# Optimization experiments

Measured on AMD Instinct MI355X. Metric: run time of the kernel, lower is better.

The kernel has to match this reference:

```python
import jax, jax.numpy as jnp
import numpy as np

N = 50000        # nodes
E = 800000       # edges (avg degree 16)
D_IN = 64
D_HID = 128      # 2 * out_dim
D_OUT = 64


def setup_inputs() -> dict:
    key = jax.random.key(0)
    ks = jax.random.split(key, 6)
    x = jax.random.normal(ks[0], (N, D_IN), dtype=jnp.float32)
    edge_index = jax.random.randint(ks[1], (2, E), 0, N, dtype=jnp.int32)
    # Glorot-style init like PyG GCNConv
    W1 = jax.random.normal(ks[2], (D_IN, D_HID), dtype=jnp.float32) / np.sqrt(D_IN)
    b1 = jnp.zeros((D_HID,), dtype=jnp.float32)
    W2 = jax.random.normal(ks[3], (D_HID, D_OUT), dtype=jnp.float32) / np.sqrt(D_HID)
    b2 = jnp.zeros((D_OUT,), dtype=jnp.float32)
    return {"x": x, "edge_index": edge_index, "W1": W1, "b1": b1, "W2": W2, "b2": b2}


def _gcn_norm(edge_index, num_nodes):
    # PyG GCNConv default: add self-loops, symmetric normalization D^-1/2 A_hat D^-1/2
    loop = jnp.arange(num_nodes, dtype=edge_index.dtype)
    src = jnp.concatenate([edge_index[0], loop])
    dst = jnp.concatenate([edge_index[1], loop])
    deg = jax.ops.segment_sum(jnp.ones_like(dst, dtype=jnp.float32), dst,
                              num_segments=num_nodes)
    dinv = jnp.where(deg > 0, jax.lax.rsqrt(deg), 0.0)
    norm = dinv[src] * dinv[dst]  # [E+N]
    return src, dst, norm


def _gcn_conv(x, W, b, src, dst, norm, num_nodes):
    h = x @ W                                      # [N, F_out]
    msg = h[src] * norm[:, None]                   # gather + scale, [E+N, F_out]
    out = jax.ops.segment_sum(msg, dst, num_segments=num_nodes)  # scatter-add
    return out + b


def reference(x, edge_index, W1, b1, W2, b2):
    num_nodes = x.shape[0]
    src, dst, norm = _gcn_norm(edge_index, num_nodes)
    h = _gcn_conv(x, W1, b1, src, dst, norm, num_nodes)
    h = jax.nn.relu(h)
    node_emb = _gcn_conv(h, W2, b2, src, dst, norm, num_nodes)
    return node_emb
```

## Files before the change

kernel.cpp:

```cpp
#include <hip/hip_runtime.h>

typedef unsigned short u16;
typedef unsigned int u32;

typedef __attribute__((ext_vector_type(8))) short bf16x8;
typedef __attribute__((ext_vector_type(4))) float f32x4;

#define BSH 8
#define CAP 5120
#define OVFCAP 8192
#define CHUNK 2048

__device__ __forceinline__ float bf2f(u16 u) {
    return __uint_as_float(((u32)u) << 16);
}
__device__ __forceinline__ u16 f2bf(float f) {
    u32 x = __float_as_uint(f);
    return (u16)((x + 0x7fffu + ((x >> 16) & 1u)) >> 16);
}

__device__ __forceinline__ bool block_isbf(const u16* __restrict__ x, float* sflag) {
    int tid = threadIdx.x;
    if (tid < 64) {
        u16 v = x[tid * 2];
        u32 ex = (v >> 7) & 0xFFu;
        unsigned long long m = __ballot(ex >= 90u && ex <= 140u);
        if (tid == 0) *sflag = (m == ~0ull) ? 1.0f : 0.0f;
    }
    __syncthreads();
    return *sflag != 0.0f;
}

__device__ __forceinline__ void acc8(uint4 w, float* a) {
    a[0] += bf2f((u16)(w.x & 0xFFFFu)); a[1] += bf2f((u16)(w.x >> 16));
    a[2] += bf2f((u16)(w.y & 0xFFFFu)); a[3] += bf2f((u16)(w.y >> 16));
    a[4] += bf2f((u16)(w.z & 0xFFFFu)); a[5] += bf2f((u16)(w.z >> 16));
    a[6] += bf2f((u16)(w.w & 0xFFFFu)); a[7] += bf2f((u16)(w.w >> 16));
}

__device__ __forceinline__ u32 scale2(u32 g, float di) {
    u16 lo = f2bf(bf2f((u16)(g & 0xFFFFu)) * di);
    u16 hi = f2bf(bf2f((u16)(g >> 16)) * di);
    return (u32)lo | ((u32)hi << 16);
}

__global__ __launch_bounds__(256) void k_binA2(
    const int* __restrict__ src, const int* __restrict__ dst,
    int* __restrict__ gcur, u32* __restrict__ staging,
    u32* __restrict__ ovf, int* __restrict__ ovfcur, int E) {
    __shared__ int hcnt[256];
    __shared__ int hbase[256];
    const int tid = threadIdx.x;
    const int e0 = blockIdx.x * CHUNK;
    const int e1 = min(e0 + CHUNK, E);
    hcnt[tid] = 0;
    __syncthreads();
    int dl[8], sl[8];
#pragma unroll
    for (int k = 0; k < 8; k++) {
        int e = e0 + tid + k * 256;
        bool ok = e < e1;
        dl[k] = ok ? dst[e] : -1;
        sl[k] = ok ? src[e] : 0;
        if (ok) atomicAdd(&hcnt[dl[k] >> BSH], 1);
    }
    __syncthreads();
    {
        int c = hcnt[tid];
        hbase[tid] = (c > 0) ? atomicAdd(&gcur[tid], c) : 0;
        hcnt[tid] = 0;
    }
    __syncthreads();
#pragma unroll
    for (int k = 0; k < 8; k++) {
        int d = dl[k];
        if (d < 0) continue;
        int b = d >> BSH;
        int r = atomicAdd(&hcnt[b], 1);
        int p = hbase[b] + r;
        if (p < CAP) {
            staging[(size_t)b * CAP + p] = (u32)sl[k] | ((u32)(d & 255) << 16);
        } else {
            int q = atomicAdd(ovfcur, 1);
            if (q < OVFCAP) ovf[q] = (u32)sl[k] | ((u32)d << 16);
        }
    }
}

__global__ __launch_bounds__(256) void k_bucket(
    const u32* __restrict__ staging, const int* __restrict__ gcur,
    const u32* __restrict__ ovf, const int* __restrict__ ovfcur,
    int* __restrict__ row_start, float* __restrict__ dinv,
    u16* __restrict__ csr, int nbuck,
    const void* __restrict__ W1, const void* __restrict__ b1,
    const void* __restrict__ W2, const void* __restrict__ b2,
    u16* __restrict__ wc,
    const void* __restrict__ x, u16* __restrict__ gxt, int N, int E) {
    __shared__ float sflag;
    __shared__ int hcnt[256];
    __shared__ int hscan[256];
    __shared__ int hcur[256];
    __shared__ int sred[256];
    __shared__ int sbase;
    __shared__ float sdinv[256];
    const int bid = blockIdx.x;
    const int tid = threadIdx.x;
    bool isbf = block_isbf((const u16*)x, &sflag);

    if (bid < nbuck) {
        const int b = bid;
        const int used = min(gcur[b], CAP);
        const u32* st = staging + (size_t)b * CAP;
        const int no = min(ovfcur[0], OVFCAP);
        const int used4 = used >> 2;
        sred[tid] = (tid < b) ? gcur[tid] : 0;
        hcnt[tid] = 0;
        __syncthreads();
        for (int s = 128; s > 0; s >>= 1) {
            if (tid < s) sred[tid] += sred[tid + s];
            __syncthreads();
        }
        if (tid == 0) sbase = sred[0];
        for (int i = tid; i < used4; i += 256) {
            uint4 p4 = ((const uint4*)st)[i];
            atomicAdd(&hcnt[p4.x >> 16], 1);
            atomicAdd(&hcnt[p4.y >> 16], 1);
            atomicAdd(&hcnt[p4.z >> 16], 1);
            atomicAdd(&hcnt[p4.w >> 16], 1);
        }
        for (int i = (used4 << 2) + tid; i < used; i += 256)
            atomicAdd(&hcnt[st[i] >> 16], 1);
        for (int i = tid; i < no; i += 256) {
            u32 pk = ovf[i];
            int d = (int)(pk >> 16);
            if ((d >> BSH) == b) atomicAdd(&hcnt[d & 255], 1);
        }
        __syncthreads();
        int v = hcnt[tid];
        hscan[tid] = v;
        __syncthreads();
        for (int s = 1; s < 256; s <<= 1) {
            int t = (tid >= s) ? hscan[tid - s] : 0;
            __syncthreads();
            hscan[tid] += t;
            __syncthreads();
        }
        int excl = hscan[tid] - v;
        hcur[tid] = excl;
        int base = sbase;
        float dv = rsqrtf((float)(v + 1));
        sdinv[tid] = dv;
        int node = (b << BSH) + tid;
        if (node < N) {
            row_start[node] = base + excl;
            dinv[node] = dv;
        }
        if (b == 0 && tid == 0) row_start[N] = E;
        __syncthreads();
        for (int i = tid; i < used4; i += 256) {
            uint4 p4 = ((const uint4*)st)[i];
            int r0 = atomicAdd(&hcur[p4.x >> 16], 1); csr[base + r0] = (u16)(p4.x & 0xFFFFu);
            int r1 = atomicAdd(&hcur[p4.y >> 16], 1); csr[base + r1] = (u16)(p4.y & 0xFFFFu);
            int r2 = atomicAdd(&hcur[p4.z >> 16], 1); csr[base + r2] = (u16)(p4.z & 0xFFFFu);
            int r3 = atomicAdd(&hcur[p4.w >> 16], 1); csr[base + r3] = (u16)(p4.w & 0xFFFFu);
        }
        for (int i = (used4 << 2) + tid; i < used; i += 256) {
            u32 pk = st[i];
            int r = atomicAdd(&hcur[pk >> 16], 1);
            csr[base + r] = (u16)(pk & 0xFFFFu);
        }
        for (int i = tid; i < no; i += 256) {
            u32 pk = ovf[i];
            int d = (int)(pk >> 16);
            if ((d >> BSH) == b) {
                int r = atomicAdd(&hcur[d & 255], 1);
                csr[base + r] = (u16)(pk & 0xFFFFu);
            }
        }
        const int row0 = b << BSH;
        for (int i = tid; i < 256 * 16; i += 256) {
            int rl = i >> 4;
            int node2 = row0 + rl;
            if (node2 >= N) break;
            int q = i & 15;
            size_t idx = (size_t)node2 * 16 + q;
            float di = sdinv[rl];
            float4 vv;
            if (isbf) {
                ushort4 u = ((const ushort4*)x)[idx];
                vv.x = bf2f(u.x); vv.y = bf2f(u.y); vv.z = bf2f(u.z); vv.w = bf2f(u.w);
            } else {
                vv = ((const float4*)x)[idx];
            }
            ushort4 o;
            o.x = f2bf(vv.x * di); o.y = f2bf(vv.y * di);
            o.z = f2bf(vv.z * di); o.w = f2bf(vv.w * di);
            ((ushort4*)gxt)[idx] = o;
        }
    } else {
        int cb = bid - nbuck;
        for (int i = cb * 256 + tid; i < 16576; i += 17 * 256) {
            const void* s; int off;
            if (i < 8192)       { int nn = i >> 6, k = i & 63;  s = W1; off = k * 128 + nn; }
            else if (i < 16384) { int j = i - 8192; int nn = j >> 7, k = j & 127; s = W2; off = k * 64 + nn; }
            else if (i < 16512) { s = b1; off = i - 16384; }
            else                { s = b2; off = i - 16512; }
            wc[i] = isbf ? ((const u16*)s)[off] : f2bf(((const float*)s)[off]);
        }
    }
}

template<bool FINAL>
__global__ __launch_bounds__(256) void k_gather(
    const uint4* __restrict__ feat, const int* __restrict__ row_start,
    const u16* __restrict__ csr, const float* __restrict__ dinv,
    const u16* __restrict__ b2c, const void* __restrict__ xdet,
    void* __restrict__ outp, int n) {
    __shared__ float sflag;
    bool isbf = true;
    if (FINAL) isbf = block_isbf((const u16*)xdet, &sflag);
    int t = blockIdx.x * 256 + threadIdx.x;
    int d = t >> 3;
    int lane = t & 7;
    if (d >= n) return;
    const uint4* fl = feat + lane;
    float a[8];
    {
        uint4 w = fl[(size_t)d * 8];
        a[0] = bf2f((u16)(w.x & 0xFFFFu)); a[1] = bf2f((u16)(w.x >> 16));
        a[2] = bf2f((u16)(w.y & 0xFFFFu)); a[3] = bf2f((u16)(w.y >> 16));
        a[4] = bf2f((u16)(w.z & 0xFFFFu)); a[5] = bf2f((u16)(w.z >> 16));
        a[6] = bf2f((u16)(w.w & 0xFFFFu)); a[7] = bf2f((u16)(w.w >> 16));
    }
    int s0 = row_start[d], s1 = row_start[d + 1];
    int deg = s1 - s0;
    int j = s0;
    int end8 = s0 + (deg & ~7);
    for (; j < end8; j += 8) {
        int idx = (int)csr[j + lane];
        uint4 wv[8];
#pragma unroll
        for (int u = 0; u < 8; u++) {
            int sv = __shfl(idx, u, 8);
            wv[u] = fl[(size_t)sv * 8];
        }
#pragma unroll
        for (int u = 0; u < 8; u++) acc8(wv[u], a);
    }
    int rem = s1 - j;
    if (rem > 0) {
        int idx = (lane < rem) ? (int)csr[j + lane] : 0;
        for (int u = 0; u < rem; u++) {
            int sv = __shfl(idx, u, 8);
            uint4 wv = fl[(size_t)sv * 8];
            acc8(wv, a);
        }
    }
    if (FINAL) {
        float di = dinv[d];
#pragma unroll
        for (int u = 0; u < 8; u++)
            a[u] = a[u] * di + bf2f(b2c[8 * lane + u]);
        if (isbf) {
            uint4 o;
            o.x = (u32)f2bf(a[0]) | ((u32)f2bf(a[1]) << 16);
            o.y = (u32)f2bf(a[2]) | ((u32)f2bf(a[3]) << 16);
            o.z = (u32)f2bf(a[4]) | ((u32)f2bf(a[5]) << 16);
            o.w = (u32)f2bf(a[6]) | ((u32)f2bf(a[7]) << 16);
            ((uint4*)outp)[(size_t)d * 8 + lane] = o;
        } else {
            float4* op = (float4*)outp;
            op[(size_t)d * 16 + 2 * lane]     = make_float4(a[0], a[1], a[2], a[3]);
            op[(size_t)d * 16 + 2 * lane + 1] = make_float4(a[4], a[5], a[6], a[7]);
        }
    } else {
        uint4 o;
        o.x = (u32)f2bf(a[0]) | ((u32)f2bf(a[1]) << 16);
        o.y = (u32)f2bf(a[2]) | ((u32)f2bf(a[3]) << 16);
        o.z = (u32)f2bf(a[4]) | ((u32)f2bf(a[5]) << 16);
        o.w = (u32)f2bf(a[6]) | ((u32)f2bf(a[7]) << 16);
        ((uint4*)outp)[(size_t)d * 8 + lane] = o;
    }
}

__global__ __launch_bounds__(256) void k_mlp(
    const u16* __restrict__ accin, const u16* __restrict__ wc,
    const float* __restrict__ dinv, u16* outb, int n) {
    __shared__ __align__(16) u16 As[32 * 72];
    __shared__ __align__(16) u16 W1t[128 * 72];
    __shared__ __align__(16) u16 W2t[64 * 136];
    __shared__ __align__(16) u16 Hs[32 * 136];
    __shared__ float b1s[128];
    __shared__ float dvs[32];
    const int tid = threadIdx.x;
    const int row0 = blockIdx.x * 32;

    if (tid < 32) {
        int r = row0 + tid;
        dvs[tid] = (r < n) ? dinv[r] : 0.f;
    } else if (tid < 160) {
        b1s[tid - 32] = bf2f(wc[16384 + tid - 32]);
    }
    {
        int i = tid;
        int r = i >> 3, kk = i & 7;
        int row = row0 + r;
        uint4 v = make_uint4(0, 0, 0, 0);
        if (row < n) {
            uint4 g = ((const uint4*)accin)[(size_t)row * 8 + kk];
            float di = dinv[row];
            v.x = scale2(g.x, di); v.y = scale2(g.y, di);
            v.z = scale2(g.z, di); v.w = scale2(g.w, di);
        }
        *(uint4*)&As[r * 72 + kk * 8] = v;
    }
    for (int i = tid; i < 1024; i += 256) {
        int nn = i >> 3, kk = i & 7;
        *(uint4*)&W1t[nn * 72 + kk * 8] = ((const uint4*)wc)[i];
    }
    for (int i = tid; i < 1024; i += 256) {
        int nn = i >> 4, kk = i & 15;
        *(uint4*)&W2t[nn * 136 + kk * 8] = ((const uint4*)(wc + 8192))[i];
    }
    __syncthreads();

    const int wave = tid >> 6;
    const int lane = tid & 63;
    const int q = lane >> 4;
    const int ln = lane & 15;

    bf16x8 a[2][2];
#pragma unroll
    for (int mt = 0; mt < 2; mt++)
#pragma unroll
        for (int ks = 0; ks < 2; ks++)
            a[mt][ks] = *(const bf16x8*)&As[(mt * 16 + ln) * 72 + ks * 32 + q * 8];

    f32x4 c1[2][2];
#pragma unroll
    for (int ntl = 0; ntl < 2; ntl++)
#pragma unroll
        for (int mt = 0; mt < 2; mt++) c1[ntl][mt] = (f32x4){0.f, 0.f, 0.f, 0.f};

#pragma unroll
    for (int ntl = 0; ntl < 2; ntl++) {
        int nt = wave * 2 + ntl;
        bf16x8 b0 = *(const bf16x8*)&W1t[(nt * 16 + ln) * 72 + 0 + q * 8];
        bf16x8 b1f = *(const bf16x8*)&W1t[(nt * 16 + ln) * 72 + 32 + q * 8];
#pragma unroll
        for (int mt = 0; mt < 2; mt++) {
            c1[ntl][mt] = __builtin_amdgcn_mfma_f32_16x16x32_bf16(a[mt][0], b0, c1[ntl][mt], 0, 0, 0);
            c1[ntl][mt] = __builtin_amdgcn_mfma_f32_16x16x32_bf16(a[mt][1], b1f, c1[ntl][mt], 0, 0, 0);
        }
    }
#pragma unroll
    for (int ntl = 0; ntl < 2; ntl++) {
        int col = (wave * 2 + ntl) * 16 + ln;
        float bb = b1s[col];
#pragma unroll
        for (int mt = 0; mt < 2; mt++)
#pragma unroll
            for (int r = 0; r < 4; r++) {
                int hrow = mt * 16 + q * 4 + r;
                Hs[hrow * 136 + col] = f2bf(fmaxf(c1[ntl][mt][r] + bb, 0.f));
            }
    }
    __syncthreads();

    f32x4 c2[2];
    c2[0] = (f32x4){0.f, 0.f, 0.f, 0.f};
    c2[1] = (f32x4){0.f, 0.f, 0.f, 0.f};
#pragma unroll
    for (int ks = 0; ks < 4; ks++) {
        bf16x8 bb = *(const bf16x8*)&W2t[(wave * 16 + ln) * 136 + ks * 32 + q * 8];
#pragma unroll
        for (int mt = 0; mt < 2; mt++) {
            bf16x8 aa = *(const bf16x8*)&Hs[(mt * 16 + ln) * 136 + ks * 32 + q * 8];
            c2[mt] = __builtin_amdgcn_mfma_f32_16x16x32_bf16(aa, bb, c2[mt], 0, 0, 0);
        }
    }
#pragma unroll
    for (int mt = 0; mt < 2; mt++)
#pragma unroll
        for (int r = 0; r < 4; r++) {
            int rloc = mt * 16 + q * 4 + r;
            int row = row0 + rloc;
            if (row < n) {
                int col = wave * 16 + ln;
                outb[(size_t)row * 64 + col] = f2bf(c2[mt][r] * dvs[rloc]);
            }
        }
}

extern "C" void kernel_launch(void* const* d_in, const int* in_sizes, int n_in,
                              void* d_out, int out_size, void* d_ws, size_t ws_size,
                              hipStream_t stream) {
    const void* x  = d_in[0];
    const int* ei  = (const int*)d_in[1];
    const void* W1 = d_in[2];
    const void* b1 = d_in[3];
    const void* W2 = d_in[4];
    const void* b2 = d_in[5];

    const int N = in_sizes[0] / 64;
    const int E = in_sizes[1] / 2;
    const int* src = ei;
    const int* dst = ei + E;

    float* ws = (float*)d_ws;
    const int NP = ((N + 64) + 63) & ~63;
    float* dinv    = ws;
    int* gcur      = (int*)(ws + NP);
    int* ovfcur    = gcur + 256;
    int* row_start = gcur + 320;
    u32* ovf       = (u32*)(row_start + ((N + 64) & ~63));
    u16* csr       = (u16*)(ovf + OVFCAP);
    u16* wc        = (u16*)(((size_t)(csr + E) + 255) & ~(size_t)255);
    u16* bufB      = (u16*)(((size_t)(wc + 16576) + 255) & ~(size_t)255);
    u32* staging   = (u32*)bufB;
    u16* gxt       = (u16*)d_out;

    const int gth = (N * 8 + 255) / 256;
    const int nbuck = (N + 255) >> BSH;
    const int binB = (E + CHUNK - 1) / CHUNK;
    dim3 blk(256);

    hipMemsetAsync(gcur, 0, 320 * sizeof(int), stream);
    k_binA2<<<dim3(binB), blk, 0, stream>>>(src, dst, gcur, staging, ovf, ovfcur, E);
    k_bucket<<<dim3(nbuck + 17), blk, 0, stream>>>(staging, gcur, ovf, ovfcur,
                                                   row_start, dinv, csr, nbuck,
                                                   W1, b1, W2, b2, wc, x, gxt, N, E);
    k_gather<false><<<dim3(gth), blk, 0, stream>>>((const uint4*)gxt, row_start, csr,
                                                   dinv, wc + 16512, x, bufB, N);
    k_mlp<<<dim3((N + 31) / 32), blk, 0, stream>>>((const u16*)bufB, wc, dinv, bufB, N);
    k_gather<true><<<dim3(gth), blk, 0, stream>>>((const uint4*)bufB, row_start, csr,
                                                  dinv, wc + 16512, x, d_out, N);
}
```

Baseline: 152.8 us.

## Vectorize edge loads, prefetch CSR indices in gather, double MLP rows per block

```diff
diff --git a/kernel.cpp b/kernel.cpp
--- a/kernel.cpp
+++ b/kernel.cpp
@@ -56,14 +56,30 @@
     hcnt[tid] = 0;
     __syncthreads();
     int dl[8], sl[8];
-#pragma unroll
-    for (int k = 0; k < 8; k++) {
-        int e = e0 + tid + k * 256;
-        bool ok = e < e1;
-        dl[k] = ok ? dst[e] : -1;
-        sl[k] = ok ? src[e] : 0;
-        if (ok) atomicAdd(&hcnt[dl[k] >> BSH], 1);
-    }
+    const int eb = e0 + tid * 8;
+    const bool vec = (eb + 7 < e1) &&
+                     ((((size_t)(dst + eb)) | ((size_t)(src + eb))) & 15) == 0;
+    if (vec) {
+        int4 d0 = ((const int4*)(dst + eb))[0];
+        int4 d1 = ((const int4*)(dst + eb))[1];
+        int4 s0v = ((const int4*)(src + eb))[0];
+        int4 s1v = ((const int4*)(src + eb))[1];
+        dl[0] = d0.x; dl[1] = d0.y; dl[2] = d0.z; dl[3] = d0.w;
+        dl[4] = d1.x; dl[5] = d1.y; dl[6] = d1.z; dl[7] = d1.w;
+        sl[0] = s0v.x; sl[1] = s0v.y; sl[2] = s0v.z; sl[3] = s0v.w;
+        sl[4] = s1v.x; sl[5] = s1v.y; sl[6] = s1v.z; sl[7] = s1v.w;
+    } else {
+#pragma unroll
+        for (int k = 0; k < 8; k++) {
+            int e = eb + k;
+            bool ok = e < e1;
+            dl[k] = ok ? dst[e] : -1;
+            sl[k] = ok ? src[e] : 0;
+        }
+    }
+#pragma unroll
+    for (int k = 0; k < 8; k++)
+        if (dl[k] >= 0) atomicAdd(&hcnt[dl[k] >> BSH], 1);
     __syncthreads();
     {
         int c = hcnt[tid];
@@ -233,25 +249,25 @@
         a[6] = bf2f((u16)(w.w & 0xFFFFu)); a[7] = bf2f((u16)(w.w >> 16));
     }
     int s0 = row_start[d], s1 = row_start[d + 1];
-    int deg = s1 - s0;
     int j = s0;
-    int end8 = s0 + (deg & ~7);
-    for (; j < end8; j += 8) {
-        int idx = (int)csr[j + lane];
+    int cur = (j + lane < s1) ? (int)csr[j + lane] : 0;
+    while (j + 8 <= s1) {
+        int nxt = (j + 8 + lane < s1) ? (int)csr[j + 8 + lane] : 0;
         uint4 wv[8];
 #pragma unroll
         for (int u = 0; u < 8; u++) {
-            int sv = __shfl(idx, u, 8);
+            int sv = __shfl(cur, u, 8);
             wv[u] = fl[(size_t)sv * 8];
         }
 #pragma unroll
         for (int u = 0; u < 8; u++) acc8(wv[u], a);
+        cur = nxt;
+        j += 8;
     }
     int rem = s1 - j;
     if (rem > 0) {
-        int idx = (lane < rem) ? (int)csr[j + lane] : 0;
         for (int u = 0; u < rem; u++) {
-            int sv = __shfl(idx, u, 8);
+            int sv = __shfl(cur, u, 8);
             uint4 wv = fl[(size_t)sv * 8];
             acc8(wv, a);
         }
@@ -286,23 +302,22 @@
 __global__ __launch_bounds__(256) void k_mlp(
     const u16* __restrict__ accin, const u16* __restrict__ wc,
     const float* __restrict__ dinv, u16* outb, int n) {
-    __shared__ __align__(16) u16 As[32 * 72];
+    __shared__ __align__(16) u16 As[64 * 72];
     __shared__ __align__(16) u16 W1t[128 * 72];
     __shared__ __align__(16) u16 W2t[64 * 136];
-    __shared__ __align__(16) u16 Hs[32 * 136];
+    __shared__ __align__(16) u16 Hs[64 * 136];
     __shared__ float b1s[128];
-    __shared__ float dvs[32];
+    __shared__ float dvs[64];
     const int tid = threadIdx.x;
-    const int row0 = blockIdx.x * 32;
-
-    if (tid < 32) {
+    const int row0 = blockIdx.x * 64;
+
+    if (tid < 64) {
         int r = row0 + tid;
         dvs[tid] = (r < n) ? dinv[r] : 0.f;
-    } else if (tid < 160) {
-        b1s[tid - 32] = bf2f(wc[16384 + tid - 32]);
-    }
-    {
-        int i = tid;
+    } else if (tid < 192) {
+        b1s[tid - 64] = bf2f(wc[16384 + tid - 64]);
+    }
+    for (int i = tid; i < 512; i += 256) {
         int r = i >> 3, kk = i & 7;
         int row = row0 + r;
         uint4 v = make_uint4(0, 0, 0, 0);
@@ -329,18 +344,18 @@
     const int q = lane >> 4;
     const int ln = lane & 15;
 
-    bf16x8 a[2][2];
-#pragma unroll
-    for (int mt = 0; mt < 2; mt++)
+    bf16x8 a[4][2];
+#pragma unroll
+    for (int mt = 0; mt < 4; mt++)
 #pragma unroll
         for (int ks = 0; ks < 2; ks++)
             a[mt][ks] = *(const bf16x8*)&As[(mt * 16 + ln) * 72 + ks * 32 + q * 8];
 
-    f32x4 c1[2][2];
+    f32x4 c1[2][4];
 #pragma unroll
     for (int ntl = 0; ntl < 2; ntl++)
 #pragma unroll
-        for (int mt = 0; mt < 2; mt++) c1[ntl][mt] = (f32x4){0.f, 0.f, 0.f, 0.f};
+        for (int mt = 0; mt < 4; mt++) c1[ntl][mt] = (f32x4){0.f, 0.f, 0.f, 0.f};
 
 #pragma unroll
     for (int ntl = 0; ntl < 2; ntl++) {
@@ -348,7 +363,7 @@
         bf16x8 b0 = *(const bf16x8*)&W1t[(nt * 16 + ln) * 72 + 0 + q * 8];
         bf16x8 b1f = *(const bf16x8*)&W1t[(nt * 16 + ln) * 72 + 32 + q * 8];
 #pragma unroll
-        for (int mt = 0; mt < 2; mt++) {
+        for (int mt = 0; mt < 4; mt++) {
             c1[ntl][mt] = __builtin_amdgcn_mfma_f32_16x16x32_bf16(a[mt][0], b0, c1[ntl][mt], 0, 0, 0);
             c1[ntl][mt] = __builtin_amdgcn_mfma_f32_16x16x32_bf16(a[mt][1], b1f, c1[ntl][mt], 0, 0, 0);
         }
@@ -358,7 +373,7 @@
         int col = (wave * 2 + ntl) * 16 + ln;
         float bb = b1s[col];
 #pragma unroll
-        for (int mt = 0; mt < 2; mt++)
+        for (int mt = 0; mt < 4; mt++)
 #pragma unroll
             for (int r = 0; r < 4; r++) {
                 int hrow = mt * 16 + q * 4 + r;
@@ -367,20 +382,20 @@
     }
     __syncthreads();
 
-    f32x4 c2[2];
-    c2[0] = (f32x4){0.f, 0.f, 0.f, 0.f};
-    c2[1] = (f32x4){0.f, 0.f, 0.f, 0.f};
+    f32x4 c2[4];
+#pragma unroll
+    for (int mt = 0; mt < 4; mt++) c2[mt] = (f32x4){0.f, 0.f, 0.f, 0.f};
 #pragma unroll
     for (int ks = 0; ks < 4; ks++) {
         bf16x8 bb = *(const bf16x8*)&W2t[(wave * 16 + ln) * 136 + ks * 32 + q * 8];
 #pragma unroll
-        for (int mt = 0; mt < 2; mt++) {
+        for (int mt = 0; mt < 4; mt++) {
             bf16x8 aa = *(const bf16x8*)&Hs[(mt * 16 + ln) * 136 + ks * 32 + q * 8];
             c2[mt] = __builtin_amdgcn_mfma_f32_16x16x32_bf16(aa, bb, c2[mt], 0, 0, 0);
         }
     }
 #pragma unroll
-    for (int mt = 0; mt < 2; mt++)
+    for (int mt = 0; mt < 4; mt++)
 #pragma unroll
         for (int r = 0; r < 4; r++) {
             int rloc = mt * 16 + q * 4 + r;
@@ -432,7 +447,7 @@
                                                    W1, b1, W2, b2, wc, x, gxt, N, E);
     k_gather<false><<<dim3(gth), blk, 0, stream>>>((const uint4*)gxt, row_start, csr,
                                                    dinv, wc + 16512, x, bufB, N);
-    k_mlp<<<dim3((N + 31) / 32), blk, 0, stream>>>((const u16*)bufB, wc, dinv, bufB, N);
+    k_mlp<<<dim3((N + 63) / 64), blk, 0, stream>>>((const u16*)bufB, wc, dinv, bufB, N);
     k_gather<true><<<dim3(gth), blk, 0, stream>>>((const uint4*)bufB, row_start, csr,
                                                   dinv, wc + 16512, x, d_out, N);
 }
```

New measurement: 150.0 us (median of 2 runs). No clear change (-1.8%).
